# Performance work log

Hardware: AMD Instinct MI355X
Metric: run time of the kernel (lower is better)

Reference implementation:

```python
import jax, jax.numpy as jnp
import numpy as np

N_HEAD = 16
HEAD_SIZE = 64
N_EMBD = 1024
B, T = 4, 2048
THETA = 10000.0


def _rope_cos_sin(t_len, dim):
    # freqs: (dim//2,), angles: (T, dim//2)
    inv = 1.0 / (THETA ** (jnp.arange(0, dim, 2, dtype=jnp.float32) / dim))
    ang = jnp.arange(t_len, dtype=jnp.float32)[:, None] * inv[None, :]
    return jnp.cos(ang), jnp.sin(ang)


def _apply_rope(x, cos, sin):
    # x: (B, H, T, hs) -> complex-pair rotation over last dim
    xr = x.reshape(*x.shape[:-1], -1, 2)
    x0, x1 = xr[..., 0], xr[..., 1]
    c = cos[None, None, :, :]
    s = sin[None, None, :, :]
    o0 = x0 * c - x1 * s
    o1 = x0 * s + x1 * c
    return jnp.stack([o0, o1], axis=-1).reshape(x.shape)


def setup_inputs() -> dict:
    key = jax.random.key(0)
    ks = jax.random.split(key, 5)
    scale = 1.0 / np.sqrt(N_EMBD)
    return {
        "x": jax.random.normal(ks[0], (B, T, N_EMBD), dtype=jnp.float32),
        "Wq": jax.random.normal(ks[1], (N_EMBD, N_HEAD * HEAD_SIZE), dtype=jnp.float32) * scale,
        "Wk": jax.random.normal(ks[2], (N_EMBD, N_HEAD * HEAD_SIZE), dtype=jnp.float32) * scale,
        "Wv": jax.random.normal(ks[3], (N_EMBD, N_HEAD * HEAD_SIZE), dtype=jnp.float32) * scale,
        "Wp": jax.random.normal(ks[4], (N_HEAD * HEAD_SIZE, N_EMBD), dtype=jnp.float32) * scale,
        "bp": jnp.zeros((N_EMBD,), dtype=jnp.float32),
    }


def reference(x, Wq, Wk, Wv, Wp, bp):
    Bx, Tx, C = x.shape
    q = (x @ Wq).reshape(Bx, Tx, N_HEAD, HEAD_SIZE).transpose(0, 2, 1, 3)
    k = (x @ Wk).reshape(Bx, Tx, N_HEAD, HEAD_SIZE).transpose(0, 2, 1, 3)
    v = (x @ Wv).reshape(Bx, Tx, N_HEAD, HEAD_SIZE).transpose(0, 2, 1, 3)
    cos, sin = _rope_cos_sin(Tx, HEAD_SIZE)
    q = _apply_rope(q, cos, sin)
    k = _apply_rope(k, cos, sin)
    wei = jnp.einsum('bhqd,bhkd->bhqk', q, k) * (HEAD_SIZE ** -0.5)
    causal = jnp.tril(jnp.ones((Tx, Tx), dtype=bool))
    wei = jnp.where(causal[None, None, :, :], wei, -jnp.inf)
    wei = jax.nn.softmax(wei, axis=-1)
    out = jnp.einsum('bhqk,bhkd->bhqd', wei, v)
    out = out.transpose(0, 2, 1, 3).reshape(Bx, Tx, N_HEAD * HEAD_SIZE)
    return out @ Wp + bp
```

## Files before the change

### kernel.cpp

```cpp
#include <hip/hip_runtime.h>
#include <hip/hip_bf16.h>

#define NH 16
#define HS 64
#define CE 1024
#define BB 4
#define TT 2048

typedef __bf16 bf16;
typedef __bf16 v8bf __attribute__((ext_vector_type(8)));
typedef __bf16 v4bf __attribute__((ext_vector_type(4)));
typedef __bf16 v2bf __attribute__((ext_vector_type(2)));
typedef float v4f __attribute__((ext_vector_type(4)));
typedef float v16f __attribute__((ext_vector_type(16)));

#define GLD16(gp, lp)                                                              \
    __builtin_amdgcn_global_load_lds((const __attribute__((address_space(1))) void*)(gp), \
                                     (__attribute__((address_space(3))) void*)(lp), 16, 0, 0)

__global__ __launch_bounds__(256) void prep_kernel(const float* __restrict__ x,
                                                   const float* __restrict__ W0,
                                                   const float* __restrict__ W1,
                                                   const float* __restrict__ W2,
                                                   const float* __restrict__ W3,
                                                   bf16* __restrict__ xb,
                                                   float2* __restrict__ csQ,
                                                   float2* __restrict__ csK,
                                                   bf16* __restrict__ dqkv,
                                                   bf16* __restrict__ dp) {
    __shared__ bf16 tile[64][66];
    const int bid = blockIdx.x;
    const int tid = threadIdx.x;
    if (bid < 4096) {
        int idx = (bid * 256 + tid) * 8;
        const float4* xp = (const float4*)(x + idx);
        float4 a = xp[0], b = xp[1];
        v8bf o;
        o[0] = (bf16)a.x; o[1] = (bf16)a.y; o[2] = (bf16)a.z; o[3] = (bf16)a.w;
        o[4] = (bf16)b.x; o[5] = (bf16)b.y; o[6] = (bf16)b.z; o[7] = (bf16)b.w;
        *(v8bf*)(xb + idx) = o;
    } else if (bid < 4352) {
        int idx = (bid - 4096) * 256 + tid;
        int t = idx >> 5, i = idx & 31;
        float inv = exp2f(-0.41524101186092034f * (float)i);
        float ang = (float)t * inv;
        float s, c;
        sincosf(ang, &s, &c);
        const float QS = 0.18033688011112042f;
        csK[idx] = make_float2(c, s);
        csQ[idx] = make_float2(c * QS, s * QS);
    } else {
        int idx = bid - 4352;
        int z = idx >> 8, rem = idx & 255;
        const float* W = (z == 0) ? W0 : (z == 1) ? W1 : (z == 2) ? W2 : W3;
        bf16* Wt = (z < 3) ? (dqkv + (size_t)z * 1024 * CE) : dp;
        int k0 = (rem & 15) * 64;
        int n0 = (rem >> 4) * 64;
        int tx = tid & 63;
        int ty = tid >> 6;
        for (int s = 0; s < 16; s++) {
            int r = s * 4 + ty;
            tile[r][tx] = (bf16)W[(size_t)(k0 + r) * CE + n0 + tx];
        }
        __syncthreads();
        for (int s = 0; s < 16; s++) {
            int r = s * 4 + ty;
            Wt[(size_t)(n0 + r) * CE + k0 + tx] = tile[tx][r];
        }
    }
}

template <int MODE>
__global__ __launch_bounds__(256) void gemm_bt(const bf16* __restrict__ A,
                                               const bf16* __restrict__ Bt,
                                               bf16* __restrict__ Qb_, bf16* __restrict__ Kb_,
                                               bf16* __restrict__ Vt_,
                                               float* __restrict__ Pout,
                                               const float* __restrict__ bias,
                                               const float2* __restrict__ csQ,
                                               const float2* __restrict__ csK) {
    __shared__ __align__(16) bf16 As[128 * 64];
    __shared__ __align__(16) bf16 Bs[128 * 64];
    const int tid = threadIdx.x;
    const int lane = tid & 63, wave = tid >> 6;
    const int lane15 = lane & 15, quad = lane >> 4;
    const int wr = wave >> 1, wc = wave & 1;
    const int m0 = blockIdx.y * 128;
    const int n0 = blockIdx.x * 128;

    v4f acc[4][4] = {};

    const int cm = tid >> 3;
    const int ck = ((tid & 7) ^ (cm & 7)) * 8;
    const bf16* Ag = A + (size_t)(m0 + cm) * CE + ck;
    const bf16* Bg = Bt + (size_t)(n0 + cm) * CE + ck;
    bf16* aD = &As[wave * 512];
    bf16* bD = &Bs[wave * 512];

    for (int k0 = 0; k0 < CE; k0 += 64) {
        __syncthreads();
#pragma unroll
        for (int p = 0; p < 4; p++) GLD16(Ag + k0 + (size_t)(p * 32) * CE, aD + p * 2048);
#pragma unroll
        for (int p = 0; p < 4; p++) GLD16(Bg + k0 + (size_t)(p * 32) * CE, bD + p * 2048);
        __syncthreads();
#pragma unroll
        for (int kh = 0; kh < 2; kh++) {
            v8bf af[4], bfr[4];
            for (int i = 0; i < 4; i++) {
                int row = wr * 64 + i * 16 + lane15;
                af[i] = *(const v8bf*)(&As[row * 64 + (((kh * 4 + quad) ^ (lane15 & 7)) * 8)]);
            }
            for (int j = 0; j < 4; j++) {
                int row = wc * 64 + j * 16 + lane15;
                bfr[j] = *(const v8bf*)(&Bs[row * 64 + (((kh * 4 + quad) ^ (lane15 & 7)) * 8)]);
            }
            for (int i = 0; i < 4; i++)
                for (int j = 0; j < 4; j++)
                    acc[i][j] = __builtin_amdgcn_mfma_f32_16x16x32_bf16(af[i], bfr[j], acc[i][j], 0, 0, 0);
        }
    }

    for (int i = 0; i < 4; i++) {
        for (int j = 0; j < 4; j++) {
            int gmb = m0 + wr * 64 + i * 16 + quad * 4;
            int gn = n0 + wc * 64 + j * 16 + lane15;
            if (MODE == 1) {
                float bb = bias[gn];
                for (int r = 0; r < 4; r++)
                    Pout[(size_t)(gmb + r) * CE + gn] = acc[i][j][r] + bb;
            } else {
                int w = gn >> 10;
                int n = gn & 1023;
                int hh = n >> 6, d = n & 63;
                if (w < 2) {
                    bf16* out = w ? Kb_ : Qb_;
                    const float2* csRow = (w ? csK : csQ) + (d >> 1);
                    for (int r = 0; r < 4; r++) {
                        int gm = gmb + r;
                        int b = gm >> 11, t = gm & 2047;
                        float xv = acc[i][j][r];
                        float pv = __shfl_xor(xv, 1);
                        float2 cs = csRow[t * 32];
                        float ov = (gn & 1) ? (pv * cs.y + xv * cs.x)
                                            : (xv * cs.x - pv * cs.y);
                        out[(((size_t)(b * NH + hh)) * TT + t) * HS + d] = (bf16)ov;
                    }
                } else {
                    int b = gmb >> 11, t = gmb & 2047;
                    v4bf pack;
                    for (int r = 0; r < 4; r++) pack[r] = (bf16)acc[i][j][r];
                    *(v4bf*)(&Vt_[(((size_t)(b * NH + hh)) * HS + d) * TT + t]) = pack;
                }
            }
        }
    }
}

__global__ __launch_bounds__(256, 4) void attn_kernel(const bf16* __restrict__ Qb,
                                                      const bf16* __restrict__ Kb,
                                                      const bf16* __restrict__ Vt,
                                                      bf16* __restrict__ Ob) {
    __shared__ __align__(16) bf16 Ks[64 * 64];
    __shared__ __align__(16) bf16 Vs[64 * 64];
    const int tid = threadIdx.x, lane = tid & 63, wave = tid >> 6;
    const int lane31 = lane & 31, h = lane >> 5;
    const int bh = blockIdx.x & 63;
    const int qb = 15 - (int)(blockIdx.x >> 6);
    const int q0 = qb * 128 + wave * 32;
    const bf16* Qp = Qb + (size_t)bh * TT * HS;
    const bf16* Kp = Kb + (size_t)bh * TT * HS;
    const bf16* Vp = Vt + (size_t)bh * HS * TT;

    v8bf qf[4];
    for (int m = 0; m < 4; m++)
        qf[m] = *(const v8bf*)(Qp + (size_t)(q0 + lane31) * HS + m * 16 + h * 8);

    v16f o0 = {}, o1 = {};
    float l_i = 0.f;

    const int kr = tid >> 3, kc = tid & 7;
    const bf16* kg = Kp + kr * HS + ((kc ^ (kr & 7)) * 8);
    const bf16* vg = Vp + (size_t)kr * TT + ((kc ^ (kr & 7)) * 8);
    bf16* ksD = &Ks[wave * 512];
    bf16* vsD = &Vs[wave * 512];

    const int kv_max = qb * 128 + 96;
    for (int kv0 = 0; kv0 <= kv_max; kv0 += 64) {
        __syncthreads();
        GLD16(kg + (size_t)kv0 * HS, ksD);
        GLD16(kg + (size_t)(kv0 + 32) * HS, ksD + 2048);
        GLD16(vg + kv0, vsD);
        GLD16(vg + kv0 + 32 * TT, vsD + 2048);
        __syncthreads();
#pragma unroll
        for (int sub = 0; sub < 2; sub++) {
            const int kvs = kv0 + sub * 32;
            if (kvs > q0) break;
            const bool diag = (kvs == q0);

            v16f s = {};
            for (int m = 0; m < 4; m++) {
                v8bf af = *(const v8bf*)(&Ks[(sub * 32 + lane31) * 64 +
                                             (((m << 1) | h) ^ (lane31 & 7)) * 8]);
                s = __builtin_amdgcn_mfma_f32_32x32x16_bf16(af, qf[m], s, 0, 0, 0);
            }

            float p[16];
            if (diag) {
                for (int r = 0; r < 16; r++) {
                    int kvr = (r & 3) + 8 * (r >> 2) + 4 * h;
                    p[r] = exp2f((kvr <= lane31) ? s[r] : -3.0e38f);
                }
            } else {
                for (int r = 0; r < 16; r++) p[r] = exp2f(s[r]);
            }
            float a8[8];
            for (int r = 0; r < 8; r++) a8[r] = p[r] + p[r + 8];
            l_i += ((a8[0] + a8[1]) + (a8[2] + a8[3])) + ((a8[4] + a8[5]) + (a8[6] + a8[7]));

            union { v4bf v; unsigned long long u; } ch[4];
            for (int g = 0; g < 4; g++)
                for (int rr = 0; rr < 4; rr++)
                    ch[g].v[rr] = (bf16)p[g * 4 + rr];

            for (int t = 0; t < 2; t++) {
                unsigned long long mine0 = ch[2 * t].u, mine1 = ch[2 * t + 1].u;
                unsigned long long send = h ? mine0 : mine1;
                unsigned long long recv = __shfl_xor(send, 32);
                union { v8bf v; unsigned long long u[2]; } bfr;
                bfr.u[0] = h ? recv : mine0;
                bfr.u[1] = h ? mine1 : recv;
                int cidx = (((sub << 2) + (t << 1) + h) ^ (lane31 & 7)) * 8;
                v8bf va0 = *(const v8bf*)(&Vs[lane31 * 64 + cidx]);
                o0 = __builtin_amdgcn_mfma_f32_32x32x16_bf16(va0, bfr.v, o0, 0, 0, 0);
                v8bf va1 = *(const v8bf*)(&Vs[(32 + lane31) * 64 + cidx]);
                o1 = __builtin_amdgcn_mfma_f32_32x32x16_bf16(va1, bfr.v, o1, 0, 0, 0);
            }
        }
    }

    const int b = bh >> 4, hh = bh & 15;
    const int q = q0 + lane31;
    float lt = l_i + __shfl_xor(l_i, 32);
    float invl = 1.f / lt;
    bf16* outRow = Ob + ((size_t)(b * TT + q)) * CE + hh * HS;
    for (int g = 0; g < 4; g++) {
        v4bf w0, w1;
        for (int rr = 0; rr < 4; rr++) {
            w0[rr] = (bf16)(o0[g * 4 + rr] * invl);
            w1[rr] = (bf16)(o1[g * 4 + rr] * invl);
        }
        *(v4bf*)(outRow + g * 8 + h * 4) = w0;
        *(v4bf*)(outRow + 32 + g * 8 + h * 4) = w1;
    }
}

extern "C" void kernel_launch(void* const* d_in, const int* in_sizes, int n_in,
                              void* d_out, int out_size, void* d_ws, size_t ws_size,
                              hipStream_t stream) {
    const float* x  = (const float*)d_in[0];
    const float* Wq = (const float*)d_in[1];
    const float* Wk = (const float*)d_in[2];
    const float* Wv = (const float*)d_in[3];
    const float* Wp = (const float*)d_in[4];
    const float* bp = (const float*)d_in[5];
    char* ws = (char*)d_ws;
    const size_t MB = 1024 * 1024;
    bf16* Xb    = (bf16*)(ws);
    bf16* WqkvT = (bf16*)(ws + 16 * MB);
    bf16* WpT   = (bf16*)(ws + 22 * MB);
    bf16* Qb    = (bf16*)(ws + 24 * MB);
    bf16* Kb    = (bf16*)(ws + 40 * MB);
    bf16* Vt    = (bf16*)(ws + 56 * MB);
    bf16* Ob    = (bf16*)(ws + 72 * MB);
    float2* csQ = (float2*)(ws + 72 * MB);
    float2* csK = (float2*)(ws + 72 * MB + 512 * 1024);

    prep_kernel<<<dim3(5376), dim3(256), 0, stream>>>(x, Wq, Wk, Wv, Wp, Xb, csQ, csK,
                                                      WqkvT, WpT);

    gemm_bt<0><<<dim3(24, 64), dim3(256), 0, stream>>>(Xb, WqkvT, Qb, Kb, Vt, nullptr, nullptr,
                                                       csQ, csK);

    attn_kernel<<<dim3(1024), dim3(256), 0, stream>>>(Qb, Kb, Vt, Ob);

    gemm_bt<1><<<dim3(8, 64), dim3(256), 0, stream>>>(Ob, WpT, nullptr, nullptr, nullptr,
                                                      (float*)d_out, bp, nullptr, nullptr);
}
```

Baseline: 258.3 us.

## Replace QKV GEMM with 256x256-tile 8-wave double-buffered pipelined kernel

Adds a new QKV projection GEMM that uses 256x256 output tiles with 8 waves, double-buffered LDS fed by direct global-to-LDS loads with XOR swizzle, and a hand-scheduled interleave of LDS reads, async loads and MFMA quarters. Explicit barriers and priority hints are placed around the MFMAs, and the block index is swizzled for L2 locality. The aim is to raise arithmetic intensity and hide memory latency relative to the old 128x128 GEMM. The cost is heavier register and LDS use (128KB LDS per block) and a fragile manual schedule.

```diff
diff --git a/kernel.cpp b/kernel.cpp
--- a/kernel.cpp
+++ b/kernel.cpp
@@ -70,6 +70,149 @@
     }
 }
 
+#define FENCE() __builtin_amdgcn_sched_barrier(0)
+#define BARRIER() { FENCE(); __builtin_amdgcn_s_barrier(); FENCE(); }
+#define LGKM0() { asm volatile("s_waitcnt lgkmcnt(0)" ::: "memory"); FENCE(); }
+#define VM6()   { asm volatile("s_waitcnt vmcnt(6)" ::: "memory"); FENCE(); }
+
+#define ST_A02(dst, kt) { GLD16(Ag + (size_t)(kt)*64,               (dst) + wv512);         \
+                          GLD16(Ag + (size_t)(kt)*64 + 2*64*CE,     (dst) + 8192 + wv512); }
+#define ST_A13(dst, kt) { GLD16(Ag + (size_t)(kt)*64 + 1*64*CE,     (dst) + 4096 + wv512);  \
+                          GLD16(Ag + (size_t)(kt)*64 + 3*64*CE,     (dst) + 12288 + wv512); }
+#define ST_B01(dst, kt) { GLD16(Bg + (size_t)(kt)*64,               (dst) + wv512);         \
+                          GLD16(Bg + (size_t)(kt)*64 + 1*64*CE,     (dst) + 4096 + wv512); }
+#define ST_B23(dst, kt) { GLD16(Bg + (size_t)(kt)*64 + 2*64*CE,     (dst) + 8192 + wv512);  \
+                          GLD16(Bg + (size_t)(kt)*64 + 3*64*CE,     (dst) + 12288 + wv512); }
+
+#define RD_A(Ab, MH) { _Pragma("unroll") for (int mi = 0; mi < 4; ++mi) {                   \
+        const int row = wr*128 + ((MH)*4+mi)*16 + lane15;                                   \
+        _Pragma("unroll") for (int kk = 0; kk < 2; ++kk)                                    \
+            af[mi][kk] = *(const v8bf*)((Ab) + row*64 + (((kk*4+quad) ^ (lane15 & 7)) * 8)); } }
+#define RD_B(Bb, NHF) { _Pragma("unroll") for (int ni = 0; ni < 2; ++ni) {                  \
+        const int nf = (NHF)*2+ni;                                                          \
+        const int row = wc*64 + nf*16 + lane15;                                             \
+        _Pragma("unroll") for (int kk = 0; kk < 2; ++kk)                                    \
+            bfq[nf][kk] = *(const v8bf*)((Bb) + row*64 + (((kk*4+quad) ^ (lane15 & 7)) * 8)); } }
+#define MM(MH, NHF) { __builtin_amdgcn_s_setprio(1);                                        \
+        _Pragma("unroll") for (int mi = 0; mi < 4; ++mi)                                    \
+        _Pragma("unroll") for (int ni = 0; ni < 2; ++ni)                                    \
+        _Pragma("unroll") for (int kk = 0; kk < 2; ++kk) {                                  \
+            const int am = (MH)*4+mi, bn = (NHF)*2+ni;                                      \
+            acc[am][bn] = __builtin_amdgcn_mfma_f32_16x16x32_bf16(af[mi][kk], bfq[bn][kk],  \
+                                                                  acc[am][bn], 0, 0, 0); }  \
+        __builtin_amdgcn_s_setprio(0); }
+
+__global__ __launch_bounds__(512, 2) void gemm_qkv8(const bf16* __restrict__ A,
+                                                    const bf16* __restrict__ Bt,
+                                                    bf16* __restrict__ Qb_,
+                                                    bf16* __restrict__ Kb_,
+                                                    bf16* __restrict__ Vt_,
+                                                    const float2* __restrict__ csQ,
+                                                    const float2* __restrict__ csK) {
+    __shared__ __align__(16) bf16 As0[16384], As1[16384], Bs0[16384], Bs1[16384];
+    const int tid = threadIdx.x;
+    const int lane = tid & 63, wave = tid >> 6;
+    const int lane15 = lane & 15, quad = lane >> 4;
+    const int wr = wave >> 2, wc = wave & 3;
+    const int wv512 = wave * 512;
+
+    const int flat = blockIdx.y * 12 + blockIdx.x;
+    const int swz = (flat & 7) * 48 + (flat >> 3);
+    const int m0 = (swz / 12) * 256;
+    const int n0 = (swz % 12) * 256;
+
+    const int srow = tid >> 3;
+    const int schk = ((tid & 7) ^ (srow & 7)) * 8;
+    const bf16* Ag = A  + (size_t)(m0 + srow) * CE + schk;
+    const bf16* Bg = Bt + (size_t)(n0 + srow) * CE + schk;
+
+    v4f acc[8][4] = {};
+    v8bf af[4][2], bfq[4][2];
+
+    ST_A02(As0, 0); ST_A13(As0, 0); ST_B01(Bs0, 0); ST_B23(Bs0, 0);
+    ST_A02(As1, 1); ST_B01(Bs1, 1); ST_A13(As1, 1);
+    VM6(); BARRIER();
+
+    for (int it = 0; it < 8; ++it) {
+        const int t = 2 * it;
+        const int tp1 = (t + 1) & 15, tp2 = (t + 2) & 15, tp3 = (t + 3) & 15;
+        RD_A(As0, 0); RD_B(Bs0, 0);
+        ST_B23(Bs1, tp1);
+        BARRIER(); LGKM0();
+        MM(0, 0);
+        BARRIER();
+        RD_B(Bs0, 1);
+        ST_A02(As0, tp2);
+        BARRIER(); LGKM0();
+        MM(0, 1);
+        BARRIER();
+        RD_A(As0, 1);
+        ST_B01(Bs0, tp2);
+        BARRIER(); LGKM0();
+        MM(1, 1);
+        BARRIER();
+        ST_A13(As0, tp2);
+        BARRIER();
+        MM(1, 0);
+        VM6();
+        BARRIER();
+        RD_A(As1, 0); RD_B(Bs1, 0);
+        ST_B23(Bs0, tp2);
+        BARRIER(); LGKM0();
+        MM(0, 0);
+        BARRIER();
+        RD_B(Bs1, 1);
+        ST_A02(As1, tp3);
+        BARRIER(); LGKM0();
+        MM(0, 1);
+        BARRIER();
+        RD_A(As1, 1);
+        ST_B01(Bs1, tp3);
+        BARRIER(); LGKM0();
+        MM(1, 1);
+        BARRIER();
+        ST_A13(As1, tp3);
+        BARRIER();
+        MM(1, 0);
+        VM6();
+        BARRIER();
+    }
+    asm volatile("s_waitcnt vmcnt(0)" ::: "memory");
+
+#pragma unroll
+    for (int m = 0; m < 8; ++m) {
+        const int gmb = m0 + wr * 128 + m * 16 + quad * 4;
+        const int bv = gmb >> 11, tq = gmb & 2047;
+#pragma unroll
+        for (int n = 0; n < 4; ++n) {
+            const int gn = n0 + wc * 64 + n * 16 + lane15;
+            const int w = gn >> 10;
+            const int nn = gn & 1023;
+            const int hh = nn >> 6, d = nn & 63;
+            if (w < 2) {
+                bf16* out = w ? Kb_ : Qb_;
+                const float2* csRow = (w ? csK : csQ) + (d >> 1);
+#pragma unroll
+                for (int r = 0; r < 4; ++r) {
+                    const int gm = gmb + r;
+                    const int b = gm >> 11, t = gm & 2047;
+                    float xv = acc[m][n][r];
+                    float pv = __shfl_xor(xv, 1);
+                    float2 cs = csRow[t * 32];
+                    float ov = (gn & 1) ? (pv * cs.y + xv * cs.x)
+                                        : (xv * cs.x - pv * cs.y);
+                    out[(((size_t)(b * NH + hh)) * TT + t) * HS + d] = (bf16)ov;
+                }
+            } else {
+                v4bf pack;
+#pragma unroll
+                for (int r = 0; r < 4; ++r) pack[r] = (bf16)acc[m][n][r];
+                *(v4bf*)(&Vt_[(((size_t)(bv * NH + hh)) * HS + d) * TT + tq]) = pack;
+            }
+        }
+    }
+}
+
 template <int MODE>
 __global__ __launch_bounds__(256) void gemm_bt(const bf16* __restrict__ A,
                                                const bf16* __restrict__ Bt,
@@ -280,8 +423,7 @@
     prep_kernel<<<dim3(5376), dim3(256), 0, stream>>>(x, Wq, Wk, Wv, Wp, Xb, csQ, csK,
                                                       WqkvT, WpT);
 
-    gemm_bt<0><<<dim3(24, 64), dim3(256), 0, stream>>>(Xb, WqkvT, Qb, Kb, Vt, nullptr, nullptr,
-                                                       csQ, csK);
+    gemm_qkv8<<<dim3(12, 32), dim3(512), 0, stream>>>(Xb, WqkvT, Qb, Kb, Vt, csQ, csK);
 
     attn_kernel<<<dim3(1024), dim3(256), 0, stream>>>(Qb, Kb, Vt, Ob);
 
```

New measurement: 273.0 us. +5.7%, slower.

## Double-buffer LDS tiles in GEMM and attention with explicit vmcnt waits

Applied to the files above, without the earlier changes.

Adds a second LDS buffer to both the projection GEMM and the attention kernel. The next K-tile (or KV-tile) is prefetched with global_load_lds while the current one is computed, and partial vmcnt waits plus raw s_barrier replace the two __syncthreads per iteration. This is meant to hide global load latency behind MFMA work. It doubles LDS use, which may lower occupancy, and it issues some extra wrapped-around prefetches at loop ends.

```diff
diff --git a/kernel.cpp b/kernel.cpp
--- a/kernel.cpp
+++ b/kernel.cpp
@@ -17,6 +17,12 @@
 #define GLD16(gp, lp)                                                              \
     __builtin_amdgcn_global_load_lds((const __attribute__((address_space(1))) void*)(gp), \
                                      (__attribute__((address_space(3))) void*)(lp), 16, 0, 0)
+
+#define FENCE() __builtin_amdgcn_sched_barrier(0)
+#define BARRIER() { FENCE(); __builtin_amdgcn_s_barrier(); FENCE(); }
+#define VM4()  { asm volatile("s_waitcnt vmcnt(4)" ::: "memory"); FENCE(); }
+#define VM8()  { asm volatile("s_waitcnt vmcnt(8)" ::: "memory"); FENCE(); }
+#define VM0()  { asm volatile("s_waitcnt vmcnt(0)" ::: "memory"); FENCE(); }
 
 __global__ __launch_bounds__(256) void prep_kernel(const float* __restrict__ x,
                                                    const float* __restrict__ W0,
@@ -70,6 +76,29 @@
     }
 }
 
+#define GSTAGE(AD, BD, kk) {                                                        \
+    _Pragma("unroll") for (int p = 0; p < 4; p++)                                   \
+        GLD16(Ag + (kk) + (size_t)(p * 32) * CE, (AD) + p * 2048);                  \
+    _Pragma("unroll") for (int p = 0; p < 4; p++)                                   \
+        GLD16(Bg + (kk) + (size_t)(p * 32) * CE, (BD) + p * 2048); }
+
+#define GCOMPUTE(ASrc, BSrc)                                                        \
+    _Pragma("unroll")                                                               \
+    for (int kh = 0; kh < 2; kh++) {                                                \
+        v8bf af[4], bfr[4];                                                         \
+        for (int i = 0; i < 4; i++) {                                               \
+            int row = wr * 64 + i * 16 + lane15;                                    \
+            af[i] = *(const v8bf*)(&ASrc[row * 64 + (((kh * 4 + quad) ^ (lane15 & 7)) * 8)]); \
+        }                                                                           \
+        for (int j = 0; j < 4; j++) {                                               \
+            int row = wc * 64 + j * 16 + lane15;                                    \
+            bfr[j] = *(const v8bf*)(&BSrc[row * 64 + (((kh * 4 + quad) ^ (lane15 & 7)) * 8)]); \
+        }                                                                           \
+        for (int i = 0; i < 4; i++)                                                 \
+            for (int j = 0; j < 4; j++)                                             \
+                acc[i][j] = __builtin_amdgcn_mfma_f32_16x16x32_bf16(af[i], bfr[j], acc[i][j], 0, 0, 0); \
+    }
+
 template <int MODE>
 __global__ __launch_bounds__(256) void gemm_bt(const bf16* __restrict__ A,
                                                const bf16* __restrict__ Bt,
@@ -79,8 +108,10 @@
                                                const float* __restrict__ bias,
                                                const float2* __restrict__ csQ,
                                                const float2* __restrict__ csK) {
-    __shared__ __align__(16) bf16 As[128 * 64];
-    __shared__ __align__(16) bf16 Bs[128 * 64];
+    __shared__ __align__(16) bf16 As0[128 * 64];
+    __shared__ __align__(16) bf16 Bs0[128 * 64];
+    __shared__ __align__(16) bf16 As1[128 * 64];
+    __shared__ __align__(16) bf16 Bs1[128 * 64];
     const int tid = threadIdx.x;
     const int lane = tid & 63, wave = tid >> 6;
     const int lane15 = lane & 15, quad = lane >> 4;
@@ -94,32 +125,23 @@
     const int ck = ((tid & 7) ^ (cm & 7)) * 8;
     const bf16* Ag = A + (size_t)(m0 + cm) * CE + ck;
     const bf16* Bg = Bt + (size_t)(n0 + cm) * CE + ck;
-    bf16* aD = &As[wave * 512];
-    bf16* bD = &Bs[wave * 512];
-
-    for (int k0 = 0; k0 < CE; k0 += 64) {
-        __syncthreads();
-#pragma unroll
-        for (int p = 0; p < 4; p++) GLD16(Ag + k0 + (size_t)(p * 32) * CE, aD + p * 2048);
-#pragma unroll
-        for (int p = 0; p < 4; p++) GLD16(Bg + k0 + (size_t)(p * 32) * CE, bD + p * 2048);
-        __syncthreads();
-#pragma unroll
-        for (int kh = 0; kh < 2; kh++) {
-            v8bf af[4], bfr[4];
-            for (int i = 0; i < 4; i++) {
-                int row = wr * 64 + i * 16 + lane15;
-                af[i] = *(const v8bf*)(&As[row * 64 + (((kh * 4 + quad) ^ (lane15 & 7)) * 8)]);
-            }
-            for (int j = 0; j < 4; j++) {
-                int row = wc * 64 + j * 16 + lane15;
-                bfr[j] = *(const v8bf*)(&Bs[row * 64 + (((kh * 4 + quad) ^ (lane15 & 7)) * 8)]);
-            }
-            for (int i = 0; i < 4; i++)
-                for (int j = 0; j < 4; j++)
-                    acc[i][j] = __builtin_amdgcn_mfma_f32_16x16x32_bf16(af[i], bfr[j], acc[i][j], 0, 0, 0);
-        }
-    }
+    bf16* aD0 = &As0[wave * 512];
+    bf16* bD0 = &Bs0[wave * 512];
+    bf16* aD1 = &As1[wave * 512];
+    bf16* bD1 = &Bs1[wave * 512];
+
+    GSTAGE(aD0, bD0, 0);
+    for (int k0 = 0; k0 < CE; k0 += 128) {
+        GSTAGE(aD1, bD1, k0 + 64);
+        VM8(); BARRIER();
+        GCOMPUTE(As0, Bs0);
+        BARRIER();
+        GSTAGE(aD0, bD0, (k0 + 128) & 1023);
+        VM8(); BARRIER();
+        GCOMPUTE(As1, Bs1);
+        BARRIER();
+    }
+    VM0();
 
     for (int i = 0; i < 4; i++) {
         for (int j = 0; j < 4; j++) {
@@ -157,12 +179,63 @@
     }
 }
 
+#define ASTAGE(KD, VD, kv) {                                        \
+    GLD16(kg + (size_t)(kv) * HS, (KD));                            \
+    GLD16(kg + (size_t)((kv) + 32) * HS, (KD) + 2048);              \
+    GLD16(vg + (kv), (VD));                                         \
+    GLD16(vg + (kv) + 32 * TT, (VD) + 2048); }
+
+#define ACOMPUTE(KS, VS, KVB)                                                       \
+    _Pragma("unroll")                                                               \
+    for (int sub = 0; sub < 2; sub++) {                                             \
+        const int kvs = (KVB) + sub * 32;                                           \
+        if (kvs > q0) break;                                                        \
+        const bool diag = (kvs == q0);                                              \
+        v16f s = {};                                                                \
+        for (int m = 0; m < 4; m++) {                                               \
+            v8bf afr = *(const v8bf*)(&KS[(sub * 32 + lane31) * 64 +                \
+                                          (((m << 1) | h) ^ (lane31 & 7)) * 8]);    \
+            s = __builtin_amdgcn_mfma_f32_32x32x16_bf16(afr, qf[m], s, 0, 0, 0);    \
+        }                                                                           \
+        float p[16];                                                                \
+        if (diag) {                                                                 \
+            for (int r = 0; r < 16; r++) {                                          \
+                int kvr = (r & 3) + 8 * (r >> 2) + 4 * h;                           \
+                p[r] = exp2f((kvr <= lane31) ? s[r] : -3.0e38f);                    \
+            }                                                                       \
+        } else {                                                                    \
+            for (int r = 0; r < 16; r++) p[r] = exp2f(s[r]);                        \
+        }                                                                           \
+        float a8[8];                                                                \
+        for (int r = 0; r < 8; r++) a8[r] = p[r] + p[r + 8];                        \
+        l_i += ((a8[0] + a8[1]) + (a8[2] + a8[3])) + ((a8[4] + a8[5]) + (a8[6] + a8[7])); \
+        union { v4bf v; unsigned long long u; } ch[4];                              \
+        for (int g = 0; g < 4; g++)                                                 \
+            for (int rr = 0; rr < 4; rr++)                                          \
+                ch[g].v[rr] = (bf16)p[g * 4 + rr];                                  \
+        for (int t2 = 0; t2 < 2; t2++) {                                            \
+            unsigned long long mine0 = ch[2 * t2].u, mine1 = ch[2 * t2 + 1].u;      \
+            unsigned long long send = h ? mine0 : mine1;                            \
+            unsigned long long recv = __shfl_xor(send, 32);                         \
+            union { v8bf v; unsigned long long u[2]; } bfr2;                        \
+            bfr2.u[0] = h ? recv : mine0;                                           \
+            bfr2.u[1] = h ? mine1 : recv;                                           \
+            int cidx = (((sub << 2) + (t2 << 1) + h) ^ (lane31 & 7)) * 8;           \
+            v8bf va0 = *(const v8bf*)(&VS[lane31 * 64 + cidx]);                     \
+            o0 = __builtin_amdgcn_mfma_f32_32x32x16_bf16(va0, bfr2.v, o0, 0, 0, 0); \
+            v8bf va1 = *(const v8bf*)(&VS[(32 + lane31) * 64 + cidx]);              \
+            o1 = __builtin_amdgcn_mfma_f32_32x32x16_bf16(va1, bfr2.v, o1, 0, 0, 0); \
+        }                                                                           \
+    }
+
 __global__ __launch_bounds__(256, 4) void attn_kernel(const bf16* __restrict__ Qb,
                                                       const bf16* __restrict__ Kb,
                                                       const bf16* __restrict__ Vt,
                                                       bf16* __restrict__ Ob) {
-    __shared__ __align__(16) bf16 Ks[64 * 64];
-    __shared__ __align__(16) bf16 Vs[64 * 64];
+    __shared__ __align__(16) bf16 Ks0[64 * 64];
+    __shared__ __align__(16) bf16 Vs0[64 * 64];
+    __shared__ __align__(16) bf16 Ks1[64 * 64];
+    __shared__ __align__(16) bf16 Vs1[64 * 64];
     const int tid = threadIdx.x, lane = tid & 63, wave = tid >> 6;
     const int lane31 = lane & 31, h = lane >> 5;
     const int bh = blockIdx.x & 63;
@@ -182,63 +255,24 @@
     const int kr = tid >> 3, kc = tid & 7;
     const bf16* kg = Kp + kr * HS + ((kc ^ (kr & 7)) * 8);
     const bf16* vg = Vp + (size_t)kr * TT + ((kc ^ (kr & 7)) * 8);
-    bf16* ksD = &Ks[wave * 512];
-    bf16* vsD = &Vs[wave * 512];
+    bf16* ksD0 = &Ks0[wave * 512];
+    bf16* vsD0 = &Vs0[wave * 512];
+    bf16* ksD1 = &Ks1[wave * 512];
+    bf16* vsD1 = &Vs1[wave * 512];
 
     const int kv_max = qb * 128 + 96;
-    for (int kv0 = 0; kv0 <= kv_max; kv0 += 64) {
-        __syncthreads();
-        GLD16(kg + (size_t)kv0 * HS, ksD);
-        GLD16(kg + (size_t)(kv0 + 32) * HS, ksD + 2048);
-        GLD16(vg + kv0, vsD);
-        GLD16(vg + kv0 + 32 * TT, vsD + 2048);
-        __syncthreads();
-#pragma unroll
-        for (int sub = 0; sub < 2; sub++) {
-            const int kvs = kv0 + sub * 32;
-            if (kvs > q0) break;
-            const bool diag = (kvs == q0);
-
-            v16f s = {};
-            for (int m = 0; m < 4; m++) {
-                v8bf af = *(const v8bf*)(&Ks[(sub * 32 + lane31) * 64 +
-                                             (((m << 1) | h) ^ (lane31 & 7)) * 8]);
-                s = __builtin_amdgcn_mfma_f32_32x32x16_bf16(af, qf[m], s, 0, 0, 0);
-            }
-
-            float p[16];
-            if (diag) {
-                for (int r = 0; r < 16; r++) {
-                    int kvr = (r & 3) + 8 * (r >> 2) + 4 * h;
-                    p[r] = exp2f((kvr <= lane31) ? s[r] : -3.0e38f);
-                }
-            } else {
-                for (int r = 0; r < 16; r++) p[r] = exp2f(s[r]);
-            }
-            float a8[8];
-            for (int r = 0; r < 8; r++) a8[r] = p[r] + p[r + 8];
-            l_i += ((a8[0] + a8[1]) + (a8[2] + a8[3])) + ((a8[4] + a8[5]) + (a8[6] + a8[7]));
-
-            union { v4bf v; unsigned long long u; } ch[4];
-            for (int g = 0; g < 4; g++)
-                for (int rr = 0; rr < 4; rr++)
-                    ch[g].v[rr] = (bf16)p[g * 4 + rr];
-
-            for (int t = 0; t < 2; t++) {
-                unsigned long long mine0 = ch[2 * t].u, mine1 = ch[2 * t + 1].u;
-                unsigned long long send = h ? mine0 : mine1;
-                unsigned long long recv = __shfl_xor(send, 32);
-                union { v8bf v; unsigned long long u[2]; } bfr;
-                bfr.u[0] = h ? recv : mine0;
-                bfr.u[1] = h ? mine1 : recv;
-                int cidx = (((sub << 2) + (t << 1) + h) ^ (lane31 & 7)) * 8;
-                v8bf va0 = *(const v8bf*)(&Vs[lane31 * 64 + cidx]);
-                o0 = __builtin_amdgcn_mfma_f32_32x32x16_bf16(va0, bfr.v, o0, 0, 0, 0);
-                v8bf va1 = *(const v8bf*)(&Vs[(32 + lane31) * 64 + cidx]);
-                o1 = __builtin_amdgcn_mfma_f32_32x32x16_bf16(va1, bfr.v, o1, 0, 0, 0);
-            }
-        }
-    }
+    ASTAGE(ksD0, vsD0, 0);
+    for (int kv0 = 0; kv0 <= kv_max; kv0 += 128) {
+        ASTAGE(ksD1, vsD1, kv0 + 64);
+        VM4(); BARRIER();
+        ACOMPUTE(Ks0, Vs0, kv0);
+        BARRIER();
+        ASTAGE(ksD0, vsD0, (kv0 + 128) & 2047);
+        VM4(); BARRIER();
+        ACOMPUTE(Ks1, Vs1, kv0 + 64);
+        BARRIER();
+    }
+    VM0();
 
     const int b = bh >> 4, hh = bh & 15;
     const int q = q0 + lane31;
```

Measured after the change: 257.0 us. No clear change (-0.5%).
